# Optimization experiments

Measured on AMD Instinct MI355X. Metric: run time of the kernel, lower is better.

## Reference

```python
import jax, jax.numpy as jnp
import numpy as np

BITS = 4
GROUPSIZE = 128
INF = 4096
OUTF = 11008
MAXQ = (1 << BITS) - 1  # 15
NGROUPS = INF // GROUPSIZE  # 32
NTOK = 256


def setup_inputs() -> dict:
    key = jax.random.key(0)
    k0, k1, k2, k3, k4 = jax.random.split(key, 5)
    imin = jnp.iinfo(jnp.int32).min
    imax = jnp.iinfo(jnp.int32).max
    x = jax.random.normal(k0, (NTOK, INF), dtype=jnp.float32)
    qweight = jax.random.randint(k1, (INF // 32 * BITS, OUTF), imin, imax, dtype=jnp.int32)
    qzeros = jax.random.randint(k2, (NGROUPS, OUTF // 32 * BITS), imin, imax, dtype=jnp.int32)
    # per-group scales: small positive values, realistic for 4-bit quant
    scales = jax.random.uniform(k3, (NGROUPS, OUTF), dtype=jnp.float32, minval=1e-3, maxval=1e-2)
    bias = jax.random.normal(k4, (OUTF,), dtype=jnp.float32)
    g_idx = (jnp.arange(INF) // GROUPSIZE).astype(jnp.int32)
    return {"x": x, "scales": scales, "bias": bias,
            "qweight": qweight, "qzeros": qzeros, "g_idx": g_idx}


def reference(x, scales, bias, qweight, qzeros, g_idx):
    # bit offsets within each packed int32 word: [0,4,8,...,28]
    wf = jnp.arange(0, 32, BITS, dtype=jnp.int32)  # [8]

    # unpack zeros: [G, OUTF//8] int32 -> [G, OUTF//8, 8] -> [G, OUTF]
    zeros = ((qzeros[:, :, None] >> wf[None, None, :]) & MAXQ) + 1
    zeros = zeros.reshape(scales.shape)  # [G, OUTF]

    # unpack weights: [INF//8, OUTF] int32 -> [INF//8, 8, OUTF] -> [INF, OUTF]
    weight = (qweight[:, None, :] >> wf[None, :, None]) & MAXQ
    weight = weight.reshape(-1, qweight.shape[1])  # [INF, OUTF]

    # group-wise dequant: w[i, o] = scales[g_idx[i], o] * (q[i, o] - zeros[g_idx[i], o])
    w = scales[g_idx] * (weight.astype(scales.dtype) - zeros[g_idx].astype(scales.dtype))

    out = jnp.matmul(x, w) + bias  # [NTOK, OUTF]
    return out
```

## Files before the change

kernel.cpp:

```cpp
#include <hip/hip_runtime.h>
#include <stdint.h>

#define INF    4096
#define OUTF   11008
#define NTOK   256
#define QZ_COLS (OUTF / 8)
#define NTILES  (INF / 128)

#define BM 64
#define BN 32

typedef __attribute__((ext_vector_type(8))) _Float16 f16x8;
typedef __attribute__((ext_vector_type(2))) _Float16 f16x2;
typedef __attribute__((ext_vector_type(4))) float    f32x4;

typedef const __attribute__((address_space(1))) uint4 gl_uint4;
typedef __attribute__((address_space(3)))       uint4 sh_uint4;

__global__ __launch_bounds__(256, 2)
void xpack(const float* __restrict__ x, uint4* __restrict__ xw)
{
    const int g  = blockIdx.x * 256 + threadIdx.x;
    const int m  = g >> 9;
    const int c8 = g & 511;
    const int t  = c8 >> 4;
    const int k8 = c8 & 15;

    const float* src = x + (size_t)m * INF + c8 * 8;
    const f32x4 v0 = *(const f32x4*)src;
    const f32x4 v1 = *(const f32x4*)(src + 4);
    uint32_t d[4];
    #pragma unroll
    for (int p = 0; p < 4; ++p)
        d[p] = __builtin_bit_cast(uint32_t, __builtin_amdgcn_cvt_pkrtz(v0[p], v1[p]));

    const int mslot = (m & 63) ^ (k8 & 7);
    const size_t oi = ((size_t)(m >> 6) * 32 + t) * 1024 + k8 * 64 + mslot;
    xw[oi] = make_uint4(d[0], d[1], d[2], d[3]);
}

__global__ __launch_bounds__(256, 6)
void qlin_mfma(const uint4* __restrict__ xw,
               const float* __restrict__ scales,
               const float* __restrict__ bias,
               const int*   __restrict__ qweight,
               const int*   __restrict__ qzeros,
               float*       __restrict__ out)
{
    __shared__ uint4 A_sh[16][64];
    __shared__ uint4 B_sh[16][32];

    const int tid   = threadIdx.x;
    const int n0    = blockIdx.x * BN;
    const int m_blk = blockIdx.y;
    const int m0    = m_blk * BM;

    const int lane = tid & 63;
    const int wid  = tid >> 6;
    const int wm   = wid >> 1;
    const int wn   = wid & 1;
    const int l15  = lane & 15;
    const int l4   = lane >> 4;

    f32x4 acc[2] = { f32x4{0.f,0.f,0.f,0.f}, f32x4{0.f,0.f,0.f,0.f} };

    const int oL  = tid & 31;
    const int bk8 = tid >> 5;
    const int zsh = (oL & 7) * 4;
    const int zcol = (n0 + oL) >> 3;

    const uint4* abase = xw + (size_t)m_blk * 32 * 1024;

    for (int t = 0; t < NTILES; ++t) {
        const uint32_t w0 = (uint32_t)qweight[(size_t)(t * 16 + bk8)     * OUTF + n0 + oL];
        const uint32_t w1 = (uint32_t)qweight[(size_t)(t * 16 + bk8 + 8) * OUTF + n0 + oL];
        const int   zw = qzeros[t * QZ_COLS + zcol];
        const float sf = scales[t * OUTF + n0 + oL];

        #pragma unroll
        for (int r = 0; r < 4; ++r) {
            const int k8 = wid * 4 + r;
            const uint4* gp = abase + (size_t)t * 1024 + k8 * 64 + lane;
            __builtin_amdgcn_global_load_lds((gl_uint4*)gp, (sh_uint4*)&A_sh[k8][0],
                                             16, 0, 0);
        }

        const int z = ((zw >> zsh) & 15) + 1;
        const _Float16 hz = (_Float16)(float)(1024 + z);
        const f16x2 z2 = {hz, hz};
        const _Float16 hs = (_Float16)sf;
        const f16x2 s2 = {hs, hs};
        uint32_t d0[4], d1[4];
        #pragma unroll
        for (int p = 0; p < 4; ++p) {
            const uint32_t b0 = ((w0 >> (4 * p)) & 0x000F000Fu) | 0x64006400u;
            const uint32_t b1 = ((w1 >> (4 * p)) & 0x000F000Fu) | 0x64006400u;
            d0[p] = __builtin_bit_cast(uint32_t,
                        (__builtin_bit_cast(f16x2, b0) - z2) * s2);
            d1[p] = __builtin_bit_cast(uint32_t,
                        (__builtin_bit_cast(f16x2, b1) - z2) * s2);
        }
        *(uint4*)&B_sh[bk8][oL]     = make_uint4(d0[0], d0[1], d0[2], d0[3]);
        *(uint4*)&B_sh[bk8 + 8][oL] = make_uint4(d1[0], d1[1], d1[2], d1[3]);

        __syncthreads();

        #pragma unroll
        for (int kk = 0; kk < 4; ++kk) {
            const int k8 = kk * 4 + l4;
            const f16x8 a0 = __builtin_bit_cast(f16x8, A_sh[k8][(wm * 32      + l15) ^ (k8 & 7)]);
            const f16x8 a1 = __builtin_bit_cast(f16x8, A_sh[k8][(wm * 32 + 16 + l15) ^ (k8 & 7)]);
            const f16x8 b  = __builtin_bit_cast(f16x8, B_sh[k8][wn * 16 + l15]);
            acc[0] = __builtin_amdgcn_mfma_f32_16x16x32_f16(a0, b, acc[0], 0, 0, 0);
            acc[1] = __builtin_amdgcn_mfma_f32_16x16x32_f16(a1, b, acc[1], 0, 0, 0);
        }

        __syncthreads();
    }

    const int col = n0 + wn * 16 + l15;
    const float bv = bias[col];
    #pragma unroll
    for (int i = 0; i < 2; ++i) {
        const int row0 = m0 + wm * 32 + i * 16 + l4 * 4;
        #pragma unroll
        for (int r = 0; r < 4; ++r)
            out[(size_t)(row0 + r) * OUTF + col] = acc[i][r] + bv;
    }
}

extern "C" void kernel_launch(void* const* d_in, const int* in_sizes, int n_in,
                              void* d_out, int out_size, void* d_ws, size_t ws_size,
                              hipStream_t stream)
{
    const float* x       = (const float*)d_in[0];
    const float* scales  = (const float*)d_in[1];
    const float* bias    = (const float*)d_in[2];
    const int*   qweight = (const int*)d_in[3];
    const int*   qzeros  = (const int*)d_in[4];
    float* out = (float*)d_out;
    uint4* xw  = (uint4*)d_ws;

    xpack<<<dim3(512), dim3(256), 0, stream>>>(x, xw);
    dim3 grid(OUTF / BN, NTOK / BM);
    qlin_mfma<<<grid, dim3(256), 0, stream>>>(xw, scales, bias, qweight, qzeros, out);
}
```

Measured before the change: 131.8 us.

## Drop LDS staging; load A and dequantized B directly into registers with prefetch

```diff
diff --git a/kernel.cpp b/kernel.cpp
--- a/kernel.cpp
+++ b/kernel.cpp
@@ -7,15 +7,9 @@
 #define QZ_COLS (OUTF / 8)
 #define NTILES  (INF / 128)
 
-#define BM 64
-#define BN 32
-
 typedef __attribute__((ext_vector_type(8))) _Float16 f16x8;
 typedef __attribute__((ext_vector_type(2))) _Float16 f16x2;
 typedef __attribute__((ext_vector_type(4))) float    f32x4;
-
-typedef const __attribute__((address_space(1))) uint4 gl_uint4;
-typedef __attribute__((address_space(3)))       uint4 sh_uint4;
 
 __global__ __launch_bounds__(256, 2)
 void xpack(const float* __restrict__ x, uint4* __restrict__ xw)
@@ -34,12 +28,67 @@
     for (int p = 0; p < 4; ++p)
         d[p] = __builtin_bit_cast(uint32_t, __builtin_amdgcn_cvt_pkrtz(v0[p], v1[p]));
 
-    const int mslot = (m & 63) ^ (k8 & 7);
-    const size_t oi = ((size_t)(m >> 6) * 32 + t) * 1024 + k8 * 64 + mslot;
+    const size_t oi = ((size_t)(m >> 6) * 32 + t) * 1024 + k8 * 64 + (m & 63);
     xw[oi] = make_uint4(d[0], d[1], d[2], d[3]);
 }
 
-__global__ __launch_bounds__(256, 6)
+
+#define ISSUE_B(S, T) do { \
+    const int _t = (T); \
+    const int* _qw = qwl + (size_t)_t * 16 * OUTF; \
+    _Pragma("unroll") for (int kk = 0; kk < 4; ++kk) { \
+        w8##S[kk * 2 + 0] = (uint32_t)_qw[(size_t)kk * 4 * OUTF]; \
+        w8##S[kk * 2 + 1] = (uint32_t)_qw[(size_t)kk * 4 * OUTF + 16]; } \
+    zwa##S = qzeros[_t * QZ_COLS + zc]; \
+    zwb##S = qzeros[_t * QZ_COLS + zc + 2]; \
+    sfa##S = scales[_t * OUTF + nw0 + l15]; \
+    sfb##S = scales[_t * OUTF + nw0 + 16 + l15]; \
+} while (0)
+
+#define LOADA(BUF, T, KK) do { \
+    const uint4* _ap = abase + (size_t)(T) * 1024 + (KK) * 256 + aoff; \
+    _Pragma("unroll") for (int i = 0; i < 4; ++i) \
+        areg##BUF[i] = __builtin_bit_cast(f16x8, _ap[i * 16]); \
+} while (0)
+
+#define TILE_BODY(CUR, NXT, T) do { \
+    const int _zA = ((zwa##CUR >> zsh) & 15) + 1; \
+    const int _zB = ((zwb##CUR >> zsh) & 15) + 1; \
+    const _Float16 _hzA = (_Float16)(float)(1024 + _zA); \
+    const _Float16 _hzB = (_Float16)(float)(1024 + _zB); \
+    const f16x2 z2a = {_hzA, _hzA}, z2b = {_hzB, _hzB}; \
+    const _Float16 _hsA = (_Float16)sfa##CUR, _hsB = (_Float16)sfb##CUR; \
+    const f16x2 s2a = {_hsA, _hsA}, s2b = {_hsB, _hsB}; \
+    LOADA(E, (T), 0); \
+    ISSUE_B(NXT, ((T) + 1 < NTILES) ? (T) + 1 : NTILES - 1); \
+    _Pragma("unroll") for (int kk = 0; kk < 4; ++kk) { \
+        if (kk == 0) LOADA(O, (T), 1); \
+        if (kk == 1) LOADA(E, (T), 2); \
+        if (kk == 2) LOADA(O, (T), 3); \
+        const uint32_t _w0 = w8##CUR[kk * 2 + 0]; \
+        const uint32_t _w1 = w8##CUR[kk * 2 + 1]; \
+        uint32_t _b0[4], _b1[4]; \
+        _Pragma("unroll") for (int p = 0; p < 4; ++p) { \
+            const uint32_t _v0 = ((_w0 >> (4 * p)) & 0x000F000Fu) | 0x64006400u; \
+            const uint32_t _v1 = ((_w1 >> (4 * p)) & 0x000F000Fu) | 0x64006400u; \
+            _b0[p] = __builtin_bit_cast(uint32_t, \
+                        (__builtin_bit_cast(f16x2, _v0) - z2a) * s2a); \
+            _b1[p] = __builtin_bit_cast(uint32_t, \
+                        (__builtin_bit_cast(f16x2, _v1) - z2b) * s2b); } \
+        const f16x8 bf0 = __builtin_bit_cast(f16x8, make_uint4(_b0[0], _b0[1], _b0[2], _b0[3])); \
+        const f16x8 bf1 = __builtin_bit_cast(f16x8, make_uint4(_b1[0], _b1[1], _b1[2], _b1[3])); \
+        _Pragma("unroll") for (int i = 0; i < 4; ++i) { \
+            if ((kk & 1) == 0) { \
+                acc[i][0] = __builtin_amdgcn_mfma_f32_16x16x32_f16(aregE[i], bf0, acc[i][0], 0, 0, 0); \
+                acc[i][1] = __builtin_amdgcn_mfma_f32_16x16x32_f16(aregE[i], bf1, acc[i][1], 0, 0, 0); \
+            } else { \
+                acc[i][0] = __builtin_amdgcn_mfma_f32_16x16x32_f16(aregO[i], bf0, acc[i][0], 0, 0, 0); \
+                acc[i][1] = __builtin_amdgcn_mfma_f32_16x16x32_f16(aregO[i], bf1, acc[i][1], 0, 0, 0); \
+            } } \
+    } \
+} while (0)
+
+__global__ __launch_bounds__(256, 2)
 void qlin_mfma(const uint4* __restrict__ xw,
                const float* __restrict__ scales,
                const float* __restrict__ bias,
@@ -47,85 +96,53 @@
                const int*   __restrict__ qzeros,
                float*       __restrict__ out)
 {
-    __shared__ uint4 A_sh[16][64];
-    __shared__ uint4 B_sh[16][32];
+    const int tid   = threadIdx.x;
+    const int m_blk = blockIdx.x;
+    const int nsup  = blockIdx.y;
+    const int wv    = tid >> 6;
+    const int lane  = tid & 63;
+    const int l15   = lane & 15;
+    const int l4    = lane >> 4;
 
-    const int tid   = threadIdx.x;
-    const int n0    = blockIdx.x * BN;
-    const int m_blk = blockIdx.y;
-    const int m0    = m_blk * BM;
+    const int nw0 = nsup * 128 + wv * 32;
+    const int m0  = m_blk * 64;
 
-    const int lane = tid & 63;
-    const int wid  = tid >> 6;
-    const int wm   = wid >> 1;
-    const int wn   = wid & 1;
-    const int l15  = lane & 15;
-    const int l4   = lane >> 4;
-
-    f32x4 acc[2] = { f32x4{0.f,0.f,0.f,0.f}, f32x4{0.f,0.f,0.f,0.f} };
-
-    const int oL  = tid & 31;
-    const int bk8 = tid >> 5;
-    const int zsh = (oL & 7) * 4;
-    const int zcol = (n0 + oL) >> 3;
-
-    const uint4* abase = xw + (size_t)m_blk * 32 * 1024;
-
-    for (int t = 0; t < NTILES; ++t) {
-        const uint32_t w0 = (uint32_t)qweight[(size_t)(t * 16 + bk8)     * OUTF + n0 + oL];
-        const uint32_t w1 = (uint32_t)qweight[(size_t)(t * 16 + bk8 + 8) * OUTF + n0 + oL];
-        const int   zw = qzeros[t * QZ_COLS + zcol];
-        const float sf = scales[t * OUTF + n0 + oL];
-
-        #pragma unroll
-        for (int r = 0; r < 4; ++r) {
-            const int k8 = wid * 4 + r;
-            const uint4* gp = abase + (size_t)t * 1024 + k8 * 64 + lane;
-            __builtin_amdgcn_global_load_lds((gl_uint4*)gp, (sh_uint4*)&A_sh[k8][0],
-                                             16, 0, 0);
-        }
-
-        const int z = ((zw >> zsh) & 15) + 1;
-        const _Float16 hz = (_Float16)(float)(1024 + z);
-        const f16x2 z2 = {hz, hz};
-        const _Float16 hs = (_Float16)sf;
-        const f16x2 s2 = {hs, hs};
-        uint32_t d0[4], d1[4];
-        #pragma unroll
-        for (int p = 0; p < 4; ++p) {
-            const uint32_t b0 = ((w0 >> (4 * p)) & 0x000F000Fu) | 0x64006400u;
-            const uint32_t b1 = ((w1 >> (4 * p)) & 0x000F000Fu) | 0x64006400u;
-            d0[p] = __builtin_bit_cast(uint32_t,
-                        (__builtin_bit_cast(f16x2, b0) - z2) * s2);
-            d1[p] = __builtin_bit_cast(uint32_t,
-                        (__builtin_bit_cast(f16x2, b1) - z2) * s2);
-        }
-        *(uint4*)&B_sh[bk8][oL]     = make_uint4(d0[0], d0[1], d0[2], d0[3]);
-        *(uint4*)&B_sh[bk8 + 8][oL] = make_uint4(d1[0], d1[1], d1[2], d1[3]);
-
-        __syncthreads();
-
-        #pragma unroll
-        for (int kk = 0; kk < 4; ++kk) {
-            const int k8 = kk * 4 + l4;
-            const f16x8 a0 = __builtin_bit_cast(f16x8, A_sh[k8][(wm * 32      + l15) ^ (k8 & 7)]);
-            const f16x8 a1 = __builtin_bit_cast(f16x8, A_sh[k8][(wm * 32 + 16 + l15) ^ (k8 & 7)]);
-            const f16x8 b  = __builtin_bit_cast(f16x8, B_sh[k8][wn * 16 + l15]);
-            acc[0] = __builtin_amdgcn_mfma_f32_16x16x32_f16(a0, b, acc[0], 0, 0, 0);
-            acc[1] = __builtin_amdgcn_mfma_f32_16x16x32_f16(a1, b, acc[1], 0, 0, 0);
-        }
-
-        __syncthreads();
+    f32x4 acc[4][2];
+    #pragma unroll
+    for (int i = 0; i < 4; ++i) {
+        acc[i][0] = f32x4{0.f, 0.f, 0.f, 0.f};
+        acc[i][1] = f32x4{0.f, 0.f, 0.f, 0.f};
     }
 
-    const int col = n0 + wn * 16 + l15;
-    const float bv = bias[col];
+    const int zsh = (l15 & 7) * 4;
+    const int zc  = (nw0 + l15) >> 3;
+    const int* qwl = qweight + (size_t)l4 * OUTF + nw0 + l15;
+    const uint4* abase = xw + (size_t)m_blk * 32 * 1024;
+    const int aoff = l4 * 64 + l15;
+
+    uint32_t w8A[8], w8B[8];
+    int zwaA, zwbA, zwaB, zwbB;
+    float sfaA, sfbA, sfaB, sfbB;
+    f16x8 aregE[4], aregO[4];
+
+    ISSUE_B(A, 0);
+
+    for (int t = 0; t < NTILES; t += 2) {
+        TILE_BODY(A, B, t);
+        TILE_BODY(B, A, t + 1);
+    }
+
     #pragma unroll
-    for (int i = 0; i < 2; ++i) {
-        const int row0 = m0 + wm * 32 + i * 16 + l4 * 4;
+    for (int j = 0; j < 2; ++j) {
+        const int col = nw0 + j * 16 + l15;
+        const float bv = bias[col];
         #pragma unroll
-        for (int r = 0; r < 4; ++r)
-            out[(size_t)(row0 + r) * OUTF + col] = acc[i][r] + bv;
+        for (int i = 0; i < 4; ++i) {
+            const int row0 = m0 + i * 16 + l4 * 4;
+            #pragma unroll
+            for (int r = 0; r < 4; ++r)
+                out[(size_t)(row0 + r) * OUTF + col] = acc[i][j][r] + bv;
+        }
     }
 }
 
@@ -142,6 +159,6 @@
     uint4* xw  = (uint4*)d_ws;
 
     xpack<<<dim3(512), dim3(256), 0, stream>>>(x, xw);
-    dim3 grid(OUTF / BN, NTOK / BM);
+    dim3 grid(4, OUTF / 128);
     qlin_mfma<<<grid, dim3(256), 0, stream>>>(xw, scales, bias, qweight, qzeros, out);
 }
```

After: 168.3 us. 27.7% more time.
